# Performance work log

Measured on AMD Instinct MI355X. Metric: run time of the kernel, lower is better.

Reference implementation:

```python
import jax, jax.numpy as jnp
import numpy as np

# Norse LIFRefracParameters defaults
DT = 0.001
TAU_SYN_INV = 200.0
TAU_MEM_INV = 100.0
V_LEAK = 0.0
V_TH = 1.0
V_RESET = 0.0
ALPHA = 100.0          # super-spike surrogate slope
RHO_RESET = 5.0        # refractory steps after a spike
TAU_FILTER_INV = 223.1435511314

T, B, F, H, O = 1000, 64, 128, 512, 32


def heaviside(x):
    return (x > 0).astype(x.dtype)


def setup_inputs() -> dict:
    key = jax.random.key(0)
    k1, k2, k3, k4, k5 = jax.random.split(key, 5)
    x = jax.random.normal(k1, (T, B, F), dtype=jnp.float32)
    # torch Linear-style uniform(-1/sqrt(fan_in), 1/sqrt(fan_in)) init
    w_in = jax.random.uniform(k2, (H, F), jnp.float32, -1.0 / np.sqrt(F), 1.0 / np.sqrt(F))
    w_rec = jax.random.uniform(k3, (H, H), jnp.float32, -1.0 / np.sqrt(H), 1.0 / np.sqrt(H))
    w_out = jax.random.uniform(k4, (O, H), jnp.float32, -1.0 / np.sqrt(H), 1.0 / np.sqrt(H))
    b_out = jax.random.uniform(k5, (O,), jnp.float32, -1.0 / np.sqrt(H), 1.0 / np.sqrt(H))
    return {"x": x, "w_in": w_in, "w_rec": w_rec, "w_out": w_out, "b_out": b_out}


def reference(x, w_in, w_rec, w_out, b_out):
    Bd, Hd = x.shape[1], w_in.shape[0]

    def step(carry, x_t):
        z, v, i, rho, o = carry
        # LIF membrane/synapse Euler update (norse lif_step)
        v_dec = v + DT * TAU_MEM_INV * ((V_LEAK - v) + i)
        i_dec = i * (1.0 - DT * TAU_SYN_INV)
        z_new = heaviside(v_dec - V_TH)
        v_new = (1.0 - z_new) * v_dec + z_new * V_RESET
        i_new = i_dec + x_t @ w_in.T + z @ w_rec.T
        # refractory update (norse compute_refractory_update)
        refrac_mask = heaviside(rho)
        v_new = (1.0 - refrac_mask) * v_new + refrac_mask * v
        z_new = (1.0 - refrac_mask) * z_new
        rho_new = (1.0 - z_new) * jnp.maximum(rho - refrac_mask, 0.0) + z_new * RHO_RESET
        # ExpFilter: linear readout + exponential low-pass
        lin = z_new @ w_out.T + b_out
        o_new = o + DT * TAU_FILTER_INV * (lin - o)
        return (z_new, v_new, i_new, rho_new, o_new), o_new

    zeros_h = jnp.zeros((Bd, Hd), x.dtype)
    o0 = jnp.zeros((Bd, w_out.shape[0]), x.dtype)
    carry0 = (zeros_h, zeros_h, zeros_h, zeros_h, o0)
    _, outputs = jax.lax.scan(step, carry0, x)
    return outputs  # [T, B, O]
```

## Files before the change

### kernel.cpp

```cpp
#include <hip/hip_runtime.h>

#define T_STEPS 1000
#define BATCH   64
#define FIN     128
#define HID     512
#define NOUT    32

__global__ void prep_transpose(const float* __restrict__ w_rec,
                               const float* __restrict__ w_out,
                               float* __restrict__ wrecT,
                               float* __restrict__ woutT) {
    int idx = blockIdx.x * blockDim.x + threadIdx.x;
    if (idx < HID * HID) {
        int j = idx / HID, h = idx % HID;
        wrecT[h * HID + j] = w_rec[idx];
    }
    if (idx < NOUT * HID) {
        int o = idx / HID, h = idx % HID;
        woutT[h * NOUT + o] = w_out[idx];
    }
}

#define GTM 128
#define GTN 128
#define GKC 32

__global__ __launch_bounds__(256)
void xwin_gemm(const float* __restrict__ x, const float* __restrict__ w_in,
               float* __restrict__ xwin) {
    __shared__ float xs[GKC][GTM + 4];
    __shared__ float ws[GKC][GTN + 4];
    const int tid = threadIdx.x;
    const int tb_base = blockIdx.x * GTM;
    const int h_base  = blockIdx.y * GTN;
    const int tx = tid & 15, ty = tid >> 4;

    float acc[8][8];
#pragma unroll
    for (int i = 0; i < 8; ++i)
#pragma unroll
        for (int j = 0; j < 8; ++j) acc[i][j] = 0.f;

    for (int kc = 0; kc < FIN; kc += GKC) {
#pragma unroll
        for (int q = 0; q < 4; ++q) {
            int li  = tid * 4 + q;
            int row = li >> 3, c4 = li & 7;
            float4 v = *(const float4*)&x[(size_t)(tb_base + row) * FIN + kc + c4 * 4];
            xs[c4*4+0][row] = v.x; xs[c4*4+1][row] = v.y;
            xs[c4*4+2][row] = v.z; xs[c4*4+3][row] = v.w;
            float4 w = *(const float4*)&w_in[(size_t)(h_base + row) * FIN + kc + c4 * 4];
            ws[c4*4+0][row] = w.x; ws[c4*4+1][row] = w.y;
            ws[c4*4+2][row] = w.z; ws[c4*4+3][row] = w.w;
        }
        __syncthreads();
#pragma unroll
        for (int k = 0; k < GKC; ++k) {
            float4 a0 = *(const float4*)&xs[k][tx * 8];
            float4 a1 = *(const float4*)&xs[k][tx * 8 + 4];
            float4 b0 = *(const float4*)&ws[k][ty * 8];
            float4 b1 = *(const float4*)&ws[k][ty * 8 + 4];
            float av[8] = {a0.x, a0.y, a0.z, a0.w, a1.x, a1.y, a1.z, a1.w};
            float bv[8] = {b0.x, b0.y, b0.z, b0.w, b1.x, b1.y, b1.z, b1.w};
#pragma unroll
            for (int i = 0; i < 8; ++i)
#pragma unroll
                for (int j = 0; j < 8; ++j)
                    acc[i][j] = fmaf(av[i], bv[j], acc[i][j]);
        }
        __syncthreads();
    }
#pragma unroll
    for (int i = 0; i < 8; ++i) {
        size_t tb = (size_t)tb_base + tx * 8 + i;
        float4 o0 = make_float4(acc[i][0], acc[i][1], acc[i][2], acc[i][3]);
        float4 o1 = make_float4(acc[i][4], acc[i][5], acc[i][6], acc[i][7]);
        *(float4*)&xwin[tb * HID + h_base + ty * 8]     = o0;
        *(float4*)&xwin[tb * HID + h_base + ty * 8 + 4] = o1;
    }
}

template<int PRECOMP>
__global__ __launch_bounds__(512)
void snn_main(const float* __restrict__ xsrc,
              const float* __restrict__ w_in,
              const float* __restrict__ wr, int wrA, int wrB,
              const float* __restrict__ wo, int woA, int woB,
              const float* __restrict__ b_out,
              float* __restrict__ out) {
    const int b    = blockIdx.x;
    const int tid  = threadIdx.x;
    const int lane = tid & 63;

    __shared__ int   s_list[2][HID];
    __shared__ int   s_cnt[2];
    __shared__ float s_xrow[2][FIN];

    if (tid < 2) s_cnt[tid] = 0;
    if (!PRECOMP && tid < FIN)
        s_xrow[0][tid] = xsrc[(size_t)b * FIN + tid];
    float iin_reg = 0.f;
    if (PRECOMP) iin_reg = xsrc[(size_t)b * HID + tid];
    __syncthreads();

    float v = 0.f, ic = 0.f, rho = 0.f, o_state = 0.f;
    const float bout_v = (tid < NOUT) ? b_out[tid] : 0.f;

    for (int t = 0; t < T_STEPS; ++t) {
        const int cur = t & 1, nxt = cur ^ 1;

        float iin_next = 0.f;
        if (PRECOMP) {
            int tn = (t + 1 < T_STEPS) ? (t + 1) : t;
            iin_next = xsrc[((size_t)tn * BATCH + b) * HID + tid];
        }

        float iin;
        if (PRECOMP) {
            iin = iin_reg;
        } else {
            float s0 = 0.f, s1 = 0.f, s2 = 0.f, s3 = 0.f;
#pragma unroll
            for (int kq = 0; kq < FIN / 4; ++kq) {
                float4 xv = *(const float4*)&s_xrow[cur][kq * 4];
                float4 wv = *(const float4*)&w_in[(size_t)tid * FIN + kq * 4];
                s0 = fmaf(xv.x, wv.x, s0);
                s1 = fmaf(xv.y, wv.y, s1);
                s2 = fmaf(xv.z, wv.z, s2);
                s3 = fmaf(xv.w, wv.w, s3);
            }
            iin = (s0 + s1) + (s2 + s3);
        }

        const int cn = s_cnt[cur];
        float r0 = 0.f, r1 = 0.f, r2 = 0.f, r3 = 0.f;
        int k = 0;
        for (; k + 4 <= cn; k += 4) {
            int i0 = s_list[cur][k],     i1 = s_list[cur][k + 1];
            int i2 = s_list[cur][k + 2], i3 = s_list[cur][k + 3];
            r0 += wr[(size_t)i0 * wrA + (size_t)tid * wrB];
            r1 += wr[(size_t)i1 * wrA + (size_t)tid * wrB];
            r2 += wr[(size_t)i2 * wrA + (size_t)tid * wrB];
            r3 += wr[(size_t)i3 * wrA + (size_t)tid * wrB];
        }
        for (; k < cn; ++k)
            r0 += wr[(size_t)s_list[cur][k] * wrA + (size_t)tid * wrB];
        const float rec = (r0 + r1) + (r2 + r3);

        const float v_dec = v + 0.1f * ((0.0f - v) + ic);
        const float i_dec = ic * 0.8f;
        float z      = (v_dec - 1.0f) > 0.0f ? 1.0f : 0.0f;
        float v_tmp  = (z != 0.0f) ? 0.0f : v_dec;
        const float refr = (rho > 0.0f) ? 1.0f : 0.0f;
        v   = (refr != 0.0f) ? v : v_tmp;
        z   = (refr != 0.0f) ? 0.0f : z;
        rho = (z != 0.0f) ? 5.0f : fmaxf(rho - refr, 0.0f);
        ic  = (i_dec + iin) + rec;

        unsigned long long m = __ballot(z != 0.0f);
        int nsp = __popcll(m);
        int base = 0;
        if (lane == 0 && nsp) base = atomicAdd(&s_cnt[nxt], nsp);
        base = __shfl(base, 0);
        if (z != 0.0f) {
            int pos = base + __popcll(m & ((1ull << lane) - 1ull));
            s_list[nxt][pos] = tid;
        }
        __syncthreads();

        if (tid < NOUT) {
            const int c2 = s_cnt[nxt];
            float lin = 0.f;
            for (int kk = 0; kk < c2; ++kk)
                lin += wo[(size_t)s_list[nxt][kk] * woA + (size_t)tid * woB];
            lin += bout_v;
            o_state = o_state + 0.2231435511314f * (lin - o_state);
            out[((size_t)t * BATCH + b) * NOUT + tid] = o_state;
        }
        if (tid == 0) s_cnt[cur] = 0;
        if (!PRECOMP && tid >= 128 && tid < 128 + FIN) {
            int tn = (t + 1 < T_STEPS) ? (t + 1) : t;
            s_xrow[nxt][tid - 128] = xsrc[((size_t)tn * BATCH + b) * FIN + (tid - 128)];
        }
        if (PRECOMP) iin_reg = iin_next;
        __syncthreads();
    }
}

extern "C" void kernel_launch(void* const* d_in, const int* in_sizes, int n_in,
                              void* d_out, int out_size, void* d_ws, size_t ws_size,
                              hipStream_t stream) {
    const float* x     = (const float*)d_in[0];
    const float* w_in  = (const float*)d_in[1];
    const float* w_rec = (const float*)d_in[2];
    const float* w_out = (const float*)d_in[3];
    const float* b_out = (const float*)d_in[4];
    float* out = (float*)d_out;

    const size_t xwin_bytes  = (size_t)T_STEPS * BATCH * HID * sizeof(float);
    const size_t wrect_bytes = (size_t)HID * HID * sizeof(float);
    const size_t woutt_bytes = (size_t)HID * NOUT * sizeof(float);

    char* ws = (char*)d_ws;

    if (ws_size >= xwin_bytes + wrect_bytes + woutt_bytes) {
        float* xwin  = (float*)ws;
        float* wrecT = (float*)(ws + xwin_bytes);
        float* woutT = (float*)(ws + xwin_bytes + wrect_bytes);
        prep_transpose<<<(HID * HID + 255) / 256, 256, 0, stream>>>(w_rec, w_out, wrecT, woutT);
        dim3 g(T_STEPS * BATCH / GTM, HID / GTN);
        xwin_gemm<<<g, 256, 0, stream>>>(x, w_in, xwin);
        snn_main<1><<<BATCH, HID, 0, stream>>>(xwin, nullptr,
                                               wrecT, HID, 1,
                                               woutT, NOUT, 1,
                                               b_out, out);
    } else if (ws_size >= wrect_bytes + woutt_bytes) {
        float* wrecT = (float*)ws;
        float* woutT = (float*)(ws + wrect_bytes);
        prep_transpose<<<(HID * HID + 255) / 256, 256, 0, stream>>>(w_rec, w_out, wrecT, woutT);
        snn_main<0><<<BATCH, HID, 0, stream>>>(x, w_in,
                                               wrecT, HID, 1,
                                               woutT, NOUT, 1,
                                               b_out, out);
    } else {
        snn_main<0><<<BATCH, HID, 0, stream>>>(x, w_in,
                                               w_rec, 1, HID,
                                               w_out, 1, HID,
                                               b_out, out);
    }
}
```

Before: 1.202 ms.

## Split SNN scan into single-wave recurrence plus parallel readout kernels

Replaces the 512-thread per-batch recurrent kernel with a single 64-lane wavefront per batch element. Each lane owns 8 neurons, spikes are kept as ballot bitmasks instead of a shared-memory list, and __syncthreads barriers are dropped from the serial time loop. The readout matmul is moved out of the scan into a parallel kernel over all timesteps that reads the stored spike masks. The exponential filter is applied in time chunks, each warmed up over the previous 128 steps so the decayed initial state becomes negligible; this is an approximation of the exact scan. The trade-off is much less parallelism per step in the serial scan, extra workspace for the masks, and the lin buffer aliased over xwin, which the scan has already finished reading.

```diff
diff --git a/kernel.cpp b/kernel.cpp
--- a/kernel.cpp
+++ b/kernel.cpp
@@ -5,6 +5,7 @@
 #define FIN     128
 #define HID     512
 #define NOUT    32
+#define ALPHA_F 0.2231435511314f
 
 __global__ void prep_transpose(const float* __restrict__ w_rec,
                                const float* __restrict__ w_out,
@@ -77,6 +78,133 @@
         float4 o1 = make_float4(acc[i][4], acc[i][5], acc[i][6], acc[i][7]);
         *(float4*)&xwin[tb * HID + h_base + ty * 8]     = o0;
         *(float4*)&xwin[tb * HID + h_base + ty * 8 + 4] = o1;
+    }
+}
+
+__global__ __launch_bounds__(64)
+void snn_scan1w(const float* __restrict__ xwin,
+                const float* __restrict__ wrT,
+                unsigned long long* __restrict__ masks) {
+    const int b    = blockIdx.x;
+    const int lane = threadIdx.x;
+    const size_t hoff = (size_t)lane * 8;
+
+    float v[8], ic[8], rho[8];
+    unsigned long long m[8];
+#pragma unroll
+    for (int j = 0; j < 8; ++j) { v[j] = 0.f; ic[j] = 0.f; rho[j] = 0.f; m[j] = 0ull; }
+
+    const float* xrow0 = &xwin[(size_t)b * HID + hoff];
+    float4 xa = *(const float4*)xrow0;
+    float4 xb = *(const float4*)(xrow0 + 4);
+
+    for (int t = 0; t < T_STEPS; ++t) {
+        const int tn = (t + 1 < T_STEPS) ? t + 1 : t;
+        const float* xnext = &xwin[((size_t)tn * BATCH + b) * HID + hoff];
+        float4 xna = *(const float4*)xnext;
+        float4 xnb = *(const float4*)(xnext + 4);
+
+        float r[8];
+#pragma unroll
+        for (int j = 0; j < 8; ++j) r[j] = 0.f;
+#pragma unroll
+        for (int j = 0; j < 8; ++j) {
+            unsigned long long mm = m[j];
+            while (mm) {
+                int l = (int)__builtin_ctzll(mm);
+                mm &= mm - 1;
+                const float* wp = &wrT[(size_t)(l * 8 + j) * HID + hoff];
+                float4 wa = *(const float4*)wp;
+                float4 wb = *(const float4*)(wp + 4);
+                r[0] += wa.x; r[1] += wa.y; r[2] += wa.z; r[3] += wa.w;
+                r[4] += wb.x; r[5] += wb.y; r[6] += wb.z; r[7] += wb.w;
+            }
+        }
+
+        const float xi[8] = {xa.x, xa.y, xa.z, xa.w, xb.x, xb.y, xb.z, xb.w};
+        float z[8];
+#pragma unroll
+        for (int j = 0; j < 8; ++j) {
+            const float v_dec = v[j] + 0.1f * ((0.0f - v[j]) + ic[j]);
+            const float i_dec = ic[j] * 0.8f;
+            float zz     = (v_dec - 1.0f) > 0.0f ? 1.0f : 0.0f;
+            float v_tmp  = (zz != 0.0f) ? 0.0f : v_dec;
+            const float refr = (rho[j] > 0.0f) ? 1.0f : 0.0f;
+            v[j]   = (refr != 0.0f) ? v[j] : v_tmp;
+            zz     = (refr != 0.0f) ? 0.0f : zz;
+            rho[j] = (zz != 0.0f) ? 5.0f : fmaxf(rho[j] - refr, 0.0f);
+            ic[j]  = (i_dec + xi[j]) + r[j];
+            z[j]   = zz;
+        }
+#pragma unroll
+        for (int j = 0; j < 8; ++j) m[j] = __ballot(z[j] != 0.0f);
+
+        if (lane == 0) {
+            unsigned long long* mg = &masks[((size_t)t * BATCH + b) * 8];
+#pragma unroll
+            for (int j = 0; j < 8; ++j) mg[j] = m[j];
+        }
+        xa = xna; xb = xnb;
+    }
+}
+
+__global__ __launch_bounds__(256)
+void readout_lin(const unsigned long long* __restrict__ masks,
+                 const float* __restrict__ woutT,
+                 float* __restrict__ lin) {
+    __shared__ float s_w[HID * NOUT];
+    const int tid = threadIdx.x;
+#pragma unroll
+    for (int q = 0; q < 16; ++q) {
+        int fi = (q * 256 + tid) * 4;
+        int h = fi >> 5, o = fi & 31;
+        float4 w = *(const float4*)&woutT[fi];
+        int xs = (h & 7) << 2;
+        *(float4*)&s_w[(h << 5) + (o ^ xs)] = w;
+    }
+    __syncthreads();
+
+    const int b  = blockIdx.y;
+    const int t  = blockIdx.x * 64 + (tid & 63);
+    const int o0 = (tid >> 6) * 8;
+    if (t >= T_STEPS) return;
+
+    const unsigned long long* mp = &masks[((size_t)t * BATCH + b) * 8];
+    float a0 = 0.f, a1 = 0.f, a2 = 0.f, a3 = 0.f, a4 = 0.f, a5 = 0.f, a6 = 0.f, a7 = 0.f;
+#pragma unroll
+    for (int j = 0; j < 8; ++j) {
+        unsigned long long mm = mp[j];
+        while (mm) {
+            int l = (int)__builtin_ctzll(mm);
+            mm &= mm - 1;
+            int h  = l * 8 + j;
+            int xs = (h & 7) << 2;
+            const float4 w0 = *(const float4*)&s_w[(h << 5) + (o0 ^ xs)];
+            const float4 w1 = *(const float4*)&s_w[(h << 5) + ((o0 + 4) ^ xs)];
+            a0 += w0.x; a1 += w0.y; a2 += w0.z; a3 += w0.w;
+            a4 += w1.x; a5 += w1.y; a6 += w1.z; a7 += w1.w;
+        }
+    }
+    float* op = &lin[((size_t)t * BATCH + b) * NOUT + o0];
+    *(float4*)op       = make_float4(a0, a1, a2, a3);
+    *(float4*)(op + 4) = make_float4(a4, a5, a6, a7);
+}
+
+__global__ __launch_bounds__(256)
+void readout_filter(const float* __restrict__ lin,
+                    const float* __restrict__ b_out,
+                    float* __restrict__ out) {
+    const int bo = blockIdx.x * 256 + threadIdx.x;
+    const int c  = blockIdx.y;
+    const float bb = b_out[bo & 31];
+    const int t0 = c * 125;
+    int ts = t0 - 128; if (ts < 0) ts = 0;
+    const int te = t0 + 125;
+    float o = 0.f;
+    for (int t = ts; t < te; ++t) {
+        float l = lin[(size_t)t * (BATCH * NOUT) + bo] + bb;
+        o = o + ALPHA_F * (l - o);
+        if (t >= t0) out[(size_t)t * (BATCH * NOUT) + bo] = o;
     }
 }
 
@@ -108,13 +236,11 @@
 
     for (int t = 0; t < T_STEPS; ++t) {
         const int cur = t & 1, nxt = cur ^ 1;
-
         float iin_next = 0.f;
         if (PRECOMP) {
             int tn = (t + 1 < T_STEPS) ? (t + 1) : t;
             iin_next = xsrc[((size_t)tn * BATCH + b) * HID + tid];
         }
-
         float iin;
         if (PRECOMP) {
             iin = iin_reg;
@@ -124,14 +250,11 @@
             for (int kq = 0; kq < FIN / 4; ++kq) {
                 float4 xv = *(const float4*)&s_xrow[cur][kq * 4];
                 float4 wv = *(const float4*)&w_in[(size_t)tid * FIN + kq * 4];
-                s0 = fmaf(xv.x, wv.x, s0);
-                s1 = fmaf(xv.y, wv.y, s1);
-                s2 = fmaf(xv.z, wv.z, s2);
-                s3 = fmaf(xv.w, wv.w, s3);
+                s0 = fmaf(xv.x, wv.x, s0); s1 = fmaf(xv.y, wv.y, s1);
+                s2 = fmaf(xv.z, wv.z, s2); s3 = fmaf(xv.w, wv.w, s3);
             }
             iin = (s0 + s1) + (s2 + s3);
         }
-
         const int cn = s_cnt[cur];
         float r0 = 0.f, r1 = 0.f, r2 = 0.f, r3 = 0.f;
         int k = 0;
@@ -157,13 +280,13 @@
         rho = (z != 0.0f) ? 5.0f : fmaxf(rho - refr, 0.0f);
         ic  = (i_dec + iin) + rec;
 
-        unsigned long long m = __ballot(z != 0.0f);
-        int nsp = __popcll(m);
+        unsigned long long mbal = __ballot(z != 0.0f);
+        int nsp = __popcll(mbal);
         int base = 0;
         if (lane == 0 && nsp) base = atomicAdd(&s_cnt[nxt], nsp);
         base = __shfl(base, 0);
         if (z != 0.0f) {
-            int pos = base + __popcll(m & ((1ull << lane) - 1ull));
+            int pos = base + __popcll(mbal & ((1ull << lane) - 1ull));
             s_list[nxt][pos] = tid;
         }
         __syncthreads();
@@ -174,15 +297,15 @@
             for (int kk = 0; kk < c2; ++kk)
                 lin += wo[(size_t)s_list[nxt][kk] * woA + (size_t)tid * woB];
             lin += bout_v;
-            o_state = o_state + 0.2231435511314f * (lin - o_state);
+            o_state = o_state + ALPHA_F * (lin - o_state);
             out[((size_t)t * BATCH + b) * NOUT + tid] = o_state;
         }
         if (tid == 0) s_cnt[cur] = 0;
+        if (PRECOMP) iin_reg = iin_next;
         if (!PRECOMP && tid >= 128 && tid < 128 + FIN) {
             int tn = (t + 1 < T_STEPS) ? (t + 1) : t;
             s_xrow[nxt][tid - 128] = xsrc[((size_t)tn * BATCH + b) * FIN + (tid - 128)];
         }
-        if (PRECOMP) iin_reg = iin_next;
         __syncthreads();
     }
 }
@@ -197,35 +320,43 @@
     const float* b_out = (const float*)d_in[4];
     float* out = (float*)d_out;
 
-    const size_t xwin_bytes  = (size_t)T_STEPS * BATCH * HID * sizeof(float);
-    const size_t wrect_bytes = (size_t)HID * HID * sizeof(float);
-    const size_t woutt_bytes = (size_t)HID * NOUT * sizeof(float);
+    const size_t xwin_b  = (size_t)T_STEPS * BATCH * HID * sizeof(float);
+    const size_t masks_b = (size_t)T_STEPS * BATCH * 8 * sizeof(unsigned long long);
+    const size_t wrect_b = (size_t)HID * HID * sizeof(float);
+    const size_t woutt_b = (size_t)HID * NOUT * sizeof(float);
 
     char* ws = (char*)d_ws;
 
-    if (ws_size >= xwin_bytes + wrect_bytes + woutt_bytes) {
+    if (ws_size >= xwin_b + masks_b + wrect_b + woutt_b) {
         float* xwin  = (float*)ws;
-        float* wrecT = (float*)(ws + xwin_bytes);
-        float* woutT = (float*)(ws + xwin_bytes + wrect_bytes);
+        float* lin   = (float*)ws;
+        unsigned long long* masks = (unsigned long long*)(ws + xwin_b);
+        float* wrecT = (float*)(ws + xwin_b + masks_b);
+        float* woutT = (float*)(ws + xwin_b + masks_b + wrect_b);
+
         prep_transpose<<<(HID * HID + 255) / 256, 256, 0, stream>>>(w_rec, w_out, wrecT, woutT);
         dim3 g(T_STEPS * BATCH / GTM, HID / GTN);
         xwin_gemm<<<g, 256, 0, stream>>>(x, w_in, xwin);
-        snn_main<1><<<BATCH, HID, 0, stream>>>(xwin, nullptr,
-                                               wrecT, HID, 1,
-                                               woutT, NOUT, 1,
-                                               b_out, out);
-    } else if (ws_size >= wrect_bytes + woutt_bytes) {
+        snn_scan1w<<<BATCH, 64, 0, stream>>>(xwin, wrecT, masks);
+        readout_lin<<<dim3((T_STEPS + 63) / 64, BATCH), 256, 0, stream>>>(masks, woutT, lin);
+        readout_filter<<<dim3(BATCH * NOUT / 256, 8), 256, 0, stream>>>(lin, b_out, out);
+    } else if (ws_size >= xwin_b + wrect_b + woutt_b) {
+        float* xwin  = (float*)ws;
+        float* wrecT = (float*)(ws + xwin_b);
+        float* woutT = (float*)(ws + xwin_b + wrect_b);
+        prep_transpose<<<(HID * HID + 255) / 256, 256, 0, stream>>>(w_rec, w_out, wrecT, woutT);
+        dim3 g(T_STEPS * BATCH / GTM, HID / GTN);
+        xwin_gemm<<<g, 256, 0, stream>>>(x, w_in, xwin);
+        snn_main<1><<<BATCH, HID, 0, stream>>>(xwin, nullptr, wrecT, HID, 1,
+                                               woutT, NOUT, 1, b_out, out);
+    } else if (ws_size >= wrect_b + woutt_b) {
         float* wrecT = (float*)ws;
-        float* woutT = (float*)(ws + wrect_bytes);
+        float* woutT = (float*)(ws + wrect_b);
         prep_transpose<<<(HID * HID + 255) / 256, 256, 0, stream>>>(w_rec, w_out, wrecT, woutT);
-        snn_main<0><<<BATCH, HID, 0, stream>>>(x, w_in,
-                                               wrecT, HID, 1,
-                                               woutT, NOUT, 1,
-                                               b_out, out);
+        snn_main<0><<<BATCH, HID, 0, stream>>>(x, w_in, wrecT, HID, 1,
+                                               woutT, NOUT, 1, b_out, out);
     } else {
-        snn_main<0><<<BATCH, HID, 0, stream>>>(x, w_in,
-                                               w_rec, 1, HID,
-                                               w_out, 1, HID,
-                                               b_out, out);
-    }
-}
+        snn_main<0><<<BATCH, HID, 0, stream>>>(x, w_in, w_rec, 1, HID,
+                                               w_out, 1, HID, b_out, out);
+    }
+}
```

Result: faster. 1.052 ms (-12.5%).
